# Kernel tuning notes

Measured on AMD Instinct MI355X. Metric: run time of the kernel, lower is better.

The kernel has to match this reference:

```python
import jax, jax.numpy as jnp
import numpy as np

R = 9  # kernal for deep=1


def setup_inputs() -> dict:
    key = jax.random.key(0)
    ks = jax.random.split(key, 9)
    B, Cin, Cout, H, W = 4, 128, 128, 360, 360
    r2 = R * R
    x = jax.random.normal(ks[0], (B, Cin, H, W), dtype=jnp.float32)
    Wconv = jax.random.normal(ks[1], (Cout, Cin), dtype=jnp.float32) * 0.05
    bconv = jax.random.normal(ks[2], (Cout,), dtype=jnp.float32) * 0.05
    Wa = jax.random.normal(ks[3], (r2, r2), dtype=jnp.float32) * 0.05
    ba = jax.random.normal(ks[4], (r2,), dtype=jnp.float32) * 0.05
    Wb = jax.random.normal(ks[5], (r2, r2), dtype=jnp.float32) * 0.05
    bb = jax.random.normal(ks[6], (r2,), dtype=jnp.float32) * 0.05
    Wc = jax.random.normal(ks[7], (r2, r2), dtype=jnp.float32) * 0.05
    bc = jax.random.normal(ks[8], (r2,), dtype=jnp.float32) * 0.05
    return {"x": x, "Wconv": Wconv, "bconv": bconv,
            "Wa": Wa, "ba": ba, "Wb": Wb, "bb": bb, "Wc": Wc, "bc": bc}


def reference(x, Wconv, bconv, Wa, ba, Wb, bb, Wc, bc):
    r = R
    # 1x1 conv == channel-mixing matmul
    x = jnp.einsum('bchw,oc->bohw', x, Wconv) + bconv[None, :, None, None]
    B, C, H, W = x.shape
    padh = (-H) % r
    padw = (-W) % r
    x = jnp.pad(x, ((0, 0), (0, 0), (0, padh), (0, padw)))
    Hp, Wp = H + padh, W + padw
    h, w = Hp // r, Wp // r
    # rearrange 'b c (ch h) (cw w) -> b c (h w) (ch cw)', ch=cw=r
    x = x.reshape(B, C, r, h, r, w).transpose(0, 1, 3, 5, 2, 4).reshape(B, C, h * w, r * r)
    a = x @ Wa.T + ba
    b = x @ Wb.T + bb
    c = x @ Wc.T + bc
    # linear-attention trick: a @ (b^T @ c); b^T@c is (r^2, r^2) per (b,c)
    y = a @ (jnp.swapaxes(b, -1, -2) @ c) / r
    # inverse rearrange 'b c (h w) (ch cw) -> b c (ch h) (cw w)'
    y = y.reshape(B, C, h, w, r, r).transpose(0, 1, 4, 2, 5, 3).reshape(B, C, Hp, Wp)
    return y[:, :, :Hp - padh, :Wp - padw]
```

## Files before the change

### kernel.cpp

```cpp
#include <hip/hip_runtime.h>
#include <hip/hip_bf16.h>

typedef float f32x4 __attribute__((ext_vector_type(4)));
typedef short s16x8 __attribute__((ext_vector_type(8)));

#define DEVI __device__ __forceinline__

DEVI unsigned short f2bf(float f) {
    return __builtin_bit_cast(unsigned short, __float2bfloat16(f));
}


__global__ __launch_bounds__(256) void k_prep(
    const float* __restrict__ W, const float* __restrict__ Wa,
    const float* __restrict__ ba, const float* __restrict__ Wb,
    const float* __restrict__ bb, const float* __restrict__ Wc,
    const float* __restrict__ bc, unsigned short* __restrict__ Wbf,
    float* __restrict__ EAT, float* __restrict__ WCAT)
{
    const int tid = threadIdx.x, bid = blockIdx.x;
    if (bid < 64) {
        const int i = bid * 256 + tid;
        Wbf[i] = f2bf(W[i]);
        return;
    }
    const int out = (bid - 64) * 256 + tid;
    const int row = out / 96, col = out % 96;
    float ea = 0.f;
    if (row <= 81 && col <= 81) {
        for (int p = 0; p < 81; ++p) {
            const float wa = (col < 81) ? Wa[p * 81 + col] : ba[p];
            const float wb = (row < 81) ? Wb[p * 81 + row] : bb[p];
            ea += wa * wb;
        }
    }
    EAT[out] = ea;
    float wc = 0.f;
    if (col < 81) {
        if (row < 81) wc = Wc[col * 81 + row];
        else if (row == 81) wc = bc[col];
    }
    WCAT[out] = wc;
}

__global__ __launch_bounds__(256, 3) void k_conv(
    const float* __restrict__ x, const unsigned short* __restrict__ Wbf,
    const float* __restrict__ bcv, unsigned short* __restrict__ XR)
{
    __shared__ __align__(16) unsigned short Xs[160 * 136];
    const int tid = threadIdx.x;
    int bid = blockIdx.x;
    const int rb = bid % 10; bid /= 10;
    const int cw = bid % 9;  bid /= 9;
    const int ch = bid % 9;  const int b = bid / 9;
    const int H0 = ch * 40 + rb * 4, w0 = cw * 40;
    const int kfeat = ch * 9 + cw;
    const int t0 = rb * 160;

    const float* xb = x + (size_t)b * 128 * 129600;
    float4 va[5][4];
#pragma unroll
    for (int ii = 0; ii < 5; ++ii) {
        const int i = tid + ii * 256;
        const int cq = i / 40, nq = i % 40;
        const int hh = nq / 10, sub = nq % 10;
        const float* p = xb + (size_t)(cq * 4) * 129600 + (size_t)(H0 + hh) * 360 + w0 + sub * 4;
        va[ii][0] = *reinterpret_cast<const float4*>(p);
        va[ii][1] = *reinterpret_cast<const float4*>(p + 129600);
        va[ii][2] = *reinterpret_cast<const float4*>(p + 2 * 129600);
        va[ii][3] = *reinterpret_cast<const float4*>(p + 3 * 129600);
    }
#pragma unroll
    for (int ii = 0; ii < 5; ++ii) {
        const int i = tid + ii * 256;
        const int cq = i / 40, nq = i % 40;
        const int hh = nq / 10, sub = nq % 10;
        const int n0 = hh * 40 + sub * 4;
        const int cs = (cq ^ ((((n0 >> 2)) & 7) << 1)) * 4;
        const float4 v0 = va[ii][0], v1 = va[ii][1], v2 = va[ii][2], v3 = va[ii][3];
        ushort4 w0v = { f2bf(v0.x), f2bf(v1.x), f2bf(v2.x), f2bf(v3.x) };
        ushort4 w1v = { f2bf(v0.y), f2bf(v1.y), f2bf(v2.y), f2bf(v3.y) };
        ushort4 w2v = { f2bf(v0.z), f2bf(v1.z), f2bf(v2.z), f2bf(v3.z) };
        ushort4 w3v = { f2bf(v0.w), f2bf(v1.w), f2bf(v2.w), f2bf(v3.w) };
        *reinterpret_cast<ushort4*>(&Xs[(n0 + 0) * 136 + cs]) = w0v;
        *reinterpret_cast<ushort4*>(&Xs[(n0 + 1) * 136 + cs]) = w1v;
        *reinterpret_cast<ushort4*>(&Xs[(n0 + 2) * 136 + cs]) = w2v;
        *reinterpret_cast<ushort4*>(&Xs[(n0 + 3) * 136 + cs]) = w3v;
    }
    __syncthreads();

    const int lane = tid & 63, wid = tid >> 6;
    const int wm = wid >> 1, wn = wid & 1;
    const int lr = lane & 15, lg = lane >> 4;

    f32x4 acc[5][4] = {};
#pragma unroll
    for (int kk = 0; kk < 4; ++kk) {
        s16x8 xa[5], wb[4];
#pragma unroll
        for (int at = 0; at < 5; ++at) {
            const int n = wm * 80 + at * 16 + lr;
            const int cqs = ((kk * 8 + lg * 2) ^ (((n >> 2) & 7) << 1)) * 4;
            xa[at] = *reinterpret_cast<const s16x8*>(&Xs[n * 136 + cqs]);
        }
#pragma unroll
        for (int bt = 0; bt < 4; ++bt)
            wb[bt] = *reinterpret_cast<const s16x8*>(
                Wbf + (wn * 64 + bt * 16 + lr) * 128 + kk * 32 + lg * 8);
#pragma unroll
        for (int at = 0; at < 5; ++at)
#pragma unroll
            for (int bt = 0; bt < 4; ++bt)
                acc[at][bt] = __builtin_amdgcn_mfma_f32_16x16x32_bf16(xa[at], wb[bt], acc[at][bt], 0, 0, 0);
    }
    __syncthreads();
#pragma unroll
    for (int bt = 0; bt < 4; ++bt) {
        const int o = wn * 64 + bt * 16 + lr;
        const float bias = bcv[o];
#pragma unroll
        for (int at = 0; at < 5; ++at) {
            const int n0 = wm * 80 + at * 16 + lg * 4;
            ushort4 hv = { f2bf(acc[at][bt][0] + bias), f2bf(acc[at][bt][1] + bias),
                           f2bf(acc[at][bt][2] + bias), f2bf(acc[at][bt][3] + bias) };
            *reinterpret_cast<ushort4*>(&Xs[o * 168 + n0]) = hv;
        }
    }
    __syncthreads();
    unsigned short* dstb = XR + (size_t)b * 128 * 129600 + (size_t)kfeat * 1600 + t0;
#pragma unroll
    for (int j = 0; j < 10; ++j) {
        const int item = tid + j * 256;
        const int o = item / 20, s2 = item % 20;
        *reinterpret_cast<s16x8*>(dstb + (size_t)o * 129600 + s2 * 8) =
            *reinterpret_cast<const s16x8*>(&Xs[o * 168 + s2 * 8]);
    }
}

__global__ __launch_bounds__(256) void k_gram(
    const unsigned short* __restrict__ XR, float* __restrict__ G2)
{
    __shared__ __align__(16) unsigned short Rs[96 * 168];
    const int tid = threadIdx.x;
    const int half = blockIdx.x & 1, bo = blockIdx.x >> 1;
    for (int i = 81 * 168 + tid; i < 96 * 168; i += 256)
        Rs[i] = (i < 82 * 168) ? (unsigned short)0x3F80 : (unsigned short)0;
    const unsigned short* Rg = XR + (size_t)bo * 129600;
    const int lane = tid & 63, wid = tid >> 6;
    const int wm = wid >> 1, wn = wid & 1;
    const int lr = lane & 15, lg = lane >> 4;
    f32x4 acc[3][3] = {};
    for (int it = 0; it < 5; ++it) {
        const int t0 = half * 800 + it * 160;
        __syncthreads();
        for (int i = tid; i < 81 * 20; i += 256) {
            const int r = i / 20, g = i % 20;
            *reinterpret_cast<s16x8*>(&Rs[r * 168 + g * 8]) =
                *reinterpret_cast<const s16x8*>(Rg + (size_t)r * 1600 + t0 + g * 8);
        }
        __syncthreads();
#pragma unroll
        for (int kk = 0; kk < 5; ++kk) {
            const int koff = kk * 32 + lg * 8;
            s16x8 af[3], bfr[3];
#pragma unroll
            for (int mt = 0; mt < 3; ++mt)
                af[mt] = *reinterpret_cast<const s16x8*>(&Rs[(wm * 48 + mt * 16 + lr) * 168 + koff]);
#pragma unroll
            for (int nt = 0; nt < 3; ++nt)
                bfr[nt] = *reinterpret_cast<const s16x8*>(&Rs[(wn * 48 + nt * 16 + lr) * 168 + koff]);
#pragma unroll
            for (int mt = 0; mt < 3; ++mt)
#pragma unroll
                for (int nt = 0; nt < 3; ++nt)
                    acc[mt][nt] = __builtin_amdgcn_mfma_f32_16x16x32_bf16(af[mt], bfr[nt], acc[mt][nt], 0, 0, 0);
        }
    }
    float* Gb = G2 + (size_t)(half * 512 + bo) * 9216;
#pragma unroll
    for (int mt = 0; mt < 3; ++mt)
#pragma unroll
        for (int nt = 0; nt < 3; ++nt)
#pragma unroll
            for (int rg = 0; rg < 4; ++rg) {
                const int row = wm * 48 + mt * 16 + lg * 4 + rg;
                const int col = wn * 48 + nt * 16 + lr;
                Gb[row * 96 + col] = acc[mt][nt][rg];
            }
}

__global__ __launch_bounds__(256) void k_small(
    const float* __restrict__ G2, const float* __restrict__ EAT,
    const float* __restrict__ WCAT, unsigned short* __restrict__ NT)
{
    __shared__ float Gs[96 * 98];
    __shared__ float Us[96 * 98];
    const int tid = threadIdx.x;
    const int bo = blockIdx.x;
    const int ty = tid >> 4, tx = tid & 15;
    const int r0 = ty * 6, q0 = tx * 6;

    const float* Gg0 = G2 + (size_t)bo * 9216;
    const float* Gg1 = G2 + (size_t)(512 + bo) * 9216;
    for (int i = tid; i < 96 * 96; i += 256) {
        const int r = i / 96, c = i % 96;
        Gs[r * 98 + c] = Gg0[i] + Gg1[i];
    }
    __syncthreads();

    {
        float acc[6][6] = {};
        for (int l = 0; l <= 81; ++l) {
            float gv[6], wv[6];
#pragma unroll
            for (int a = 0; a < 6; ++a) gv[a] = Gs[l * 98 + r0 + a];
#pragma unroll
            for (int b2 = 0; b2 < 6; ++b2) wv[b2] = WCAT[l * 96 + q0 + b2];
#pragma unroll
            for (int a = 0; a < 6; ++a)
#pragma unroll
                for (int b2 = 0; b2 < 6; ++b2)
                    acc[a][b2] += gv[a] * wv[b2];
        }
#pragma unroll
        for (int a = 0; a < 6; ++a)
#pragma unroll
            for (int b2 = 0; b2 < 6; ++b2)
                Us[(r0 + a) * 98 + q0 + b2] = acc[a][b2];
    }
    __syncthreads();

    float acc[6][6] = {};
    for (int j = 0; j <= 81; ++j) {
        float ev[6], uv[6];
#pragma unroll
        for (int a = 0; a < 6; ++a) ev[a] = EAT[j * 96 + r0 + a];
#pragma unroll
        for (int b2 = 0; b2 < 6; ++b2) uv[b2] = Us[j * 98 + q0 + b2];
#pragma unroll
        for (int a = 0; a < 6; ++a)
#pragma unroll
            for (int b2 = 0; b2 < 6; ++b2)
                acc[a][b2] += ev[a] * uv[b2];
    }
    unsigned short* NTb = NT + (size_t)bo * 9216;
#pragma unroll
    for (int b2 = 0; b2 < 6; ++b2)
#pragma unroll
        for (int a = 0; a < 6; ++a)
            NTb[(q0 + b2) * 96 + (r0 + a)] = f2bf(acc[a][b2] * (1.f / 9.f));
}

__global__ __launch_bounds__(256) void k_apply(
    const unsigned short* __restrict__ XR, const unsigned short* __restrict__ NT,
    float* __restrict__ out)
{
    __shared__ __align__(16) unsigned short Xs[160 * 128];
    const int tid = threadIdx.x;
    const int fifth = blockIdx.x % 5, bo = blockIdx.x / 5;
    for (int i = tid; i < 320; i += 256) {
        const int t = i >> 1, h = i & 1;
        const int s = (t >> 3) & 7;
        const ushort4 z = { 0, 0, 0, 0 };
        if (h == 0) {
            *reinterpret_cast<ushort4*>(&Xs[t * 128 + ((10 ^ s) << 3) + 4]) = z;
        } else {
            *reinterpret_cast<ushort4*>(&Xs[t * 128 + ((11 ^ s) << 3)]) = z;
            *reinterpret_cast<ushort4*>(&Xs[t * 128 + ((11 ^ s) << 3) + 4]) = z;
        }
    }
    const int lane = tid & 63, wid = tid >> 6;
    const int wm = wid >> 1, wn = wid & 1;
    const int lr = lane & 15, lg = lane >> 4;

    const unsigned short* NTb = NT + (size_t)bo * 9216;
    s16x8 nb[3][3];
#pragma unroll
    for (int qt = 0; qt < 3; ++qt)
#pragma unroll
        for (int kk = 0; kk < 3; ++kk)
            nb[qt][kk] = *reinterpret_cast<const s16x8*>(
                NTb + (wn * 48 + qt * 16 + lr) * 96 + kk * 32 + lg * 8);

    const unsigned short* Rg = XR + (size_t)bo * 129600;
    float* ob = out + (size_t)bo * 129600;

    for (int it = 0; it < 2; ++it) {
        const int t0 = fifth * 320 + it * 160;
        __syncthreads();
        for (int i = tid; i < 420; i += 256) {
            const int kq = i / 20, g = i % 20;
            if (kq < 20) {
                const unsigned short* src = Rg + (size_t)(4 * kq) * 1600 + t0 + g * 8;
                const s16x8 v0 = *reinterpret_cast<const s16x8*>(src);
                const s16x8 v1 = *reinterpret_cast<const s16x8*>(src + 1600);
                const s16x8 v2 = *reinterpret_cast<const s16x8*>(src + 3200);
                const s16x8 v3 = *reinterpret_cast<const s16x8*>(src + 4800);
                const int colb = (((kq >> 1) ^ (g & 7)) << 3) + ((kq & 1) << 2);
#pragma unroll
                for (int e = 0; e < 8; ++e) {
                    const int t = g * 8 + e;
                    ushort4 wv = { (unsigned short)v0[e], (unsigned short)v1[e],
                                   (unsigned short)v2[e], (unsigned short)v3[e] };
                    *reinterpret_cast<ushort4*>(&Xs[t * 128 + colb]) = wv;
                }
            } else {
                const s16x8 v = *reinterpret_cast<const s16x8*>(
                    Rg + (size_t)80 * 1600 + t0 + g * 8);
                const int colb = (10 ^ (g & 7)) << 3;
#pragma unroll
                for (int e = 0; e < 8; ++e) {
                    const int t = g * 8 + e;
                    ushort4 wv = { (unsigned short)v[e], (unsigned short)0x3F80, 0, 0 };
                    *reinterpret_cast<ushort4*>(&Xs[t * 128 + colb]) = wv;
                }
            }
        }
        __syncthreads();
        f32x4 acc[5][3] = {};
#pragma unroll
        for (int kk = 0; kk < 3; ++kk) {
            s16x8 xa[5];
#pragma unroll
            for (int at = 0; at < 5; ++at) {
                const int t = wm * 80 + at * 16 + lr;
                const int s = (t >> 3) & 7;
                xa[at] = *reinterpret_cast<const s16x8*>(
                    &Xs[t * 128 + (((kk * 4 + lg) ^ s) << 3)]);
            }
#pragma unroll
            for (int at = 0; at < 5; ++at)
#pragma unroll
                for (int qt = 0; qt < 3; ++qt)
                    acc[at][qt] = __builtin_amdgcn_mfma_f32_16x16x32_bf16(xa[at], nb[qt][kk], acc[at][qt], 0, 0, 0);
        }
#pragma unroll
        for (int qt = 0; qt < 3; ++qt) {
            const int q = wn * 48 + qt * 16 + lr;
            if (q < 81) {
                const int chq = q / 9, cwq = q % 9;
                float* oq = ob + (size_t)chq * 40 * 360 + cwq * 40;
#pragma unroll
                for (int at = 0; at < 5; ++at) {
                    const int tt = t0 + wm * 80 + at * 16 + lg * 4;
                    const int hh = tt / 40, ww = tt % 40;
                    *reinterpret_cast<f32x4*>(&oq[hh * 360 + ww]) = acc[at][qt];
                }
            }
        }
    }
}

extern "C" void kernel_launch(void* const* d_in, const int* in_sizes, int n_in,
                              void* d_out, int out_size, void* d_ws, size_t ws_size,
                              hipStream_t stream)
{
    (void)in_sizes; (void)n_in; (void)out_size; (void)ws_size;
    const float* x   = (const float*)d_in[0];
    const float* Wcv = (const float*)d_in[1];
    const float* bcv = (const float*)d_in[2];
    const float* Wa  = (const float*)d_in[3];
    const float* ba  = (const float*)d_in[4];
    const float* Wb  = (const float*)d_in[5];
    const float* bbv = (const float*)d_in[6];
    const float* Wc  = (const float*)d_in[7];
    const float* bc2 = (const float*)d_in[8];
    float* out = (float*)d_out;

    char* w = (char*)d_ws;
    unsigned short* XR = (unsigned short*)w;
    float* G2 = (float*)(w + 132710400ull);
    unsigned short* NT = (unsigned short*)(w + 170459136ull);
    unsigned short* Wbf = (unsigned short*)(w + 179896320ull);
    float* EAT  = (float*)(w + 179929088ull);
    float* WCAT = (float*)(w + 179965952ull);

    k_prep <<<100,  256, 0, stream>>>(Wcv, Wa, ba, Wb, bbv, Wc, bc2, Wbf, EAT, WCAT);
    k_conv <<<3240, 256, 0, stream>>>(x, Wbf, bcv, XR);
    k_gram <<<1024, 256, 0, stream>>>(XR, G2);
    k_small<<<512,  256, 0, stream>>>(G2, EAT, WCAT, NT);
    k_apply<<<2560, 256, 0, stream>>>(XR, NT, out);
}
```

Before: 305.5 us.

## Software-pipeline global loads in conv and apply kernels with register prefetch

k_conv now processes two row-blocks per workgroup and issues the second block's global loads before computing the first, halving the grid and lowering occupancy to 2 waves per SIMD. k_apply processes five 160-column tiles per block instead of two, with a register double-buffer that prefetches the next tile's XR data while MFMAs run on the current one. The aim is to hide global memory latency behind compute. The cost is higher register pressure and fewer blocks, which can reduce latency hiding from occupancy.

```diff
diff --git a/kernel.cpp b/kernel.cpp
--- a/kernel.cpp
+++ b/kernel.cpp
@@ -43,22 +43,8 @@
     WCAT[out] = wc;
 }
 
-__global__ __launch_bounds__(256, 3) void k_conv(
-    const float* __restrict__ x, const unsigned short* __restrict__ Wbf,
-    const float* __restrict__ bcv, unsigned short* __restrict__ XR)
-{
-    __shared__ __align__(16) unsigned short Xs[160 * 136];
-    const int tid = threadIdx.x;
-    int bid = blockIdx.x;
-    const int rb = bid % 10; bid /= 10;
-    const int cw = bid % 9;  bid /= 9;
-    const int ch = bid % 9;  const int b = bid / 9;
-    const int H0 = ch * 40 + rb * 4, w0 = cw * 40;
-    const int kfeat = ch * 9 + cw;
-    const int t0 = rb * 160;
-
-    const float* xb = x + (size_t)b * 128 * 129600;
-    float4 va[5][4];
+DEVI void conv_issue(const float* xb, int H0, int w0, int tid, float4 (&va)[5][4])
+{
 #pragma unroll
     for (int ii = 0; ii < 5; ++ii) {
         const int i = tid + ii * 256;
@@ -70,6 +56,10 @@
         va[ii][2] = *reinterpret_cast<const float4*>(p + 2 * 129600);
         va[ii][3] = *reinterpret_cast<const float4*>(p + 3 * 129600);
     }
+}
+
+DEVI void conv_stage(const float4 (&va)[5][4], unsigned short* Xs, int tid)
+{
 #pragma unroll
     for (int ii = 0; ii < 5; ++ii) {
         const int i = tid + ii * 256;
@@ -87,8 +77,11 @@
         *reinterpret_cast<ushort4*>(&Xs[(n0 + 2) * 136 + cs]) = w2v;
         *reinterpret_cast<ushort4*>(&Xs[(n0 + 3) * 136 + cs]) = w3v;
     }
-    __syncthreads();
-
+}
+
+DEVI void conv_compute_store(unsigned short* Xs, const unsigned short* __restrict__ Wbf,
+                             const float* __restrict__ bcv, unsigned short* dstb, int tid)
+{
     const int lane = tid & 63, wid = tid >> 6;
     const int wm = wid >> 1, wn = wid & 1;
     const int lr = lane & 15, lg = lane >> 4;
@@ -127,7 +120,6 @@
         }
     }
     __syncthreads();
-    unsigned short* dstb = XR + (size_t)b * 128 * 129600 + (size_t)kfeat * 1600 + t0;
 #pragma unroll
     for (int j = 0; j < 10; ++j) {
         const int item = tid + j * 256;
@@ -135,6 +127,37 @@
         *reinterpret_cast<s16x8*>(dstb + (size_t)o * 129600 + s2 * 8) =
             *reinterpret_cast<const s16x8*>(&Xs[o * 168 + s2 * 8]);
     }
+    __syncthreads();
+}
+
+__global__ __launch_bounds__(256, 2) void k_conv(
+    const float* __restrict__ x, const unsigned short* __restrict__ Wbf,
+    const float* __restrict__ bcv, unsigned short* __restrict__ XR)
+{
+    __shared__ __align__(16) unsigned short Xs[160 * 136];
+    const int tid = threadIdx.x;
+    int bid = blockIdx.x;
+    const int rb2 = bid % 5; bid /= 5;
+    const int cw = bid % 9;  bid /= 9;
+    const int ch = bid % 9;  const int b = bid / 9;
+    const int w0 = cw * 40;
+    const int kfeat = ch * 9 + cw;
+    const int rb0 = rb2 * 2;
+    const int H0a = ch * 40 + rb0 * 4;
+
+    const float* xb = x + (size_t)b * 128 * 129600;
+    unsigned short* dst0 = XR + (size_t)(b * 128) * 129600 + (size_t)kfeat * 1600;
+
+    float4 va[5][4], vb[5][4];
+    conv_issue(xb, H0a, w0, tid, va);
+    conv_stage(va, Xs, tid);
+    __syncthreads();
+    conv_issue(xb, H0a + 4, w0, tid, vb);
+    conv_compute_store(Xs, Wbf, bcv, dst0 + rb0 * 160, tid);
+
+    conv_stage(vb, Xs, tid);
+    __syncthreads();
+    conv_compute_store(Xs, Wbf, bcv, dst0 + (rb0 + 1) * 160, tid);
 }
 
 __global__ __launch_bounds__(256) void k_gram(
@@ -251,13 +274,77 @@
             NTb[(q0 + b2) * 96 + (r0 + a)] = f2bf(acc[a][b2] * (1.f / 9.f));
 }
 
+DEVI void apply_issue(const unsigned short* Rg, int t0, int tid, s16x8 (&pf)[2][4])
+{
+    {
+        const int kq = tid / 20, g = tid % 20;
+        const unsigned short* src = Rg + (size_t)(4 * kq) * 1600 + t0 + g * 8;
+        pf[0][0] = *reinterpret_cast<const s16x8*>(src);
+        pf[0][1] = *reinterpret_cast<const s16x8*>(src + 1600);
+        pf[0][2] = *reinterpret_cast<const s16x8*>(src + 3200);
+        pf[0][3] = *reinterpret_cast<const s16x8*>(src + 4800);
+    }
+    if (tid < 164) {
+        const int item = tid + 256;
+        const int kq = item / 20, g = item % 20;
+        if (kq < 20) {
+            const unsigned short* src = Rg + (size_t)(4 * kq) * 1600 + t0 + g * 8;
+            pf[1][0] = *reinterpret_cast<const s16x8*>(src);
+            pf[1][1] = *reinterpret_cast<const s16x8*>(src + 1600);
+            pf[1][2] = *reinterpret_cast<const s16x8*>(src + 3200);
+            pf[1][3] = *reinterpret_cast<const s16x8*>(src + 4800);
+        } else {
+            pf[1][0] = *reinterpret_cast<const s16x8*>(
+                Rg + (size_t)80 * 1600 + t0 + g * 8);
+        }
+    }
+}
+
+DEVI void apply_stage(int tid, const s16x8 (&pf)[2][4], unsigned short* Xs)
+{
+    {
+        const int kq = tid / 20, g = tid % 20;
+        const int colb = (((kq >> 1) ^ (g & 7)) << 3) + ((kq & 1) << 2);
+#pragma unroll
+        for (int e = 0; e < 8; ++e) {
+            const int t = g * 8 + e;
+            ushort4 wv = { (unsigned short)pf[0][0][e], (unsigned short)pf[0][1][e],
+                           (unsigned short)pf[0][2][e], (unsigned short)pf[0][3][e] };
+            *reinterpret_cast<ushort4*>(&Xs[t * 128 + colb]) = wv;
+        }
+    }
+    if (tid < 164) {
+        const int item = tid + 256;
+        const int kq = item / 20, g = item % 20;
+        if (kq < 20) {
+            const int colb = (((kq >> 1) ^ (g & 7)) << 3) + ((kq & 1) << 2);
+#pragma unroll
+            for (int e = 0; e < 8; ++e) {
+                const int t = g * 8 + e;
+                ushort4 wv = { (unsigned short)pf[1][0][e], (unsigned short)pf[1][1][e],
+                               (unsigned short)pf[1][2][e], (unsigned short)pf[1][3][e] };
+                *reinterpret_cast<ushort4*>(&Xs[t * 128 + colb]) = wv;
+            }
+        } else {
+            const int colb = (10 ^ (g & 7)) << 3;
+#pragma unroll
+            for (int e = 0; e < 8; ++e) {
+                const int t = g * 8 + e;
+                ushort4 wv = { (unsigned short)pf[1][0][e], (unsigned short)0x3F80, 0, 0 };
+                *reinterpret_cast<ushort4*>(&Xs[t * 128 + colb]) = wv;
+            }
+        }
+    }
+}
+
 __global__ __launch_bounds__(256) void k_apply(
     const unsigned short* __restrict__ XR, const unsigned short* __restrict__ NT,
     float* __restrict__ out)
 {
     __shared__ __align__(16) unsigned short Xs[160 * 128];
     const int tid = threadIdx.x;
-    const int fifth = blockIdx.x % 5, bo = blockIdx.x / 5;
+    const int half = blockIdx.x & 1, bo = blockIdx.x >> 1;
+    const int t00 = half * 800;
     for (int i = tid; i < 320; i += 256) {
         const int t = i >> 1, h = i & 1;
         const int s = (t >> 3) & 7;
@@ -285,38 +372,16 @@
     const unsigned short* Rg = XR + (size_t)bo * 129600;
     float* ob = out + (size_t)bo * 129600;
 
-    for (int it = 0; it < 2; ++it) {
-        const int t0 = fifth * 320 + it * 160;
+    s16x8 pf[2][2][4];
+    apply_issue(Rg, t00, tid, pf[0]);
+
+#pragma unroll
+    for (int it = 0; it < 5; ++it) {
+        const int t0 = t00 + it * 160;
+        apply_stage(tid, pf[it & 1], Xs);
         __syncthreads();
-        for (int i = tid; i < 420; i += 256) {
-            const int kq = i / 20, g = i % 20;
-            if (kq < 20) {
-                const unsigned short* src = Rg + (size_t)(4 * kq) * 1600 + t0 + g * 8;
-                const s16x8 v0 = *reinterpret_cast<const s16x8*>(src);
-                const s16x8 v1 = *reinterpret_cast<const s16x8*>(src + 1600);
-                const s16x8 v2 = *reinterpret_cast<const s16x8*>(src + 3200);
-                const s16x8 v3 = *reinterpret_cast<const s16x8*>(src + 4800);
-                const int colb = (((kq >> 1) ^ (g & 7)) << 3) + ((kq & 1) << 2);
-#pragma unroll
-                for (int e = 0; e < 8; ++e) {
-                    const int t = g * 8 + e;
-                    ushort4 wv = { (unsigned short)v0[e], (unsigned short)v1[e],
-                                   (unsigned short)v2[e], (unsigned short)v3[e] };
-                    *reinterpret_cast<ushort4*>(&Xs[t * 128 + colb]) = wv;
-                }
-            } else {
-                const s16x8 v = *reinterpret_cast<const s16x8*>(
-                    Rg + (size_t)80 * 1600 + t0 + g * 8);
-                const int colb = (10 ^ (g & 7)) << 3;
-#pragma unroll
-                for (int e = 0; e < 8; ++e) {
-                    const int t = g * 8 + e;
-                    ushort4 wv = { (unsigned short)v[e], (unsigned short)0x3F80, 0, 0 };
-                    *reinterpret_cast<ushort4*>(&Xs[t * 128 + colb]) = wv;
-                }
-            }
-        }
-        __syncthreads();
+        if (it < 4)
+            apply_issue(Rg, t0 + 160, tid, pf[(it & 1) ^ 1]);
         f32x4 acc[5][3] = {};
 #pragma unroll
         for (int kk = 0; kk < 3; ++kk) {
@@ -348,6 +413,7 @@
                 }
             }
         }
+        __syncthreads();
     }
 }
 
@@ -376,8 +442,8 @@
     float* WCAT = (float*)(w + 179965952ull);
 
     k_prep <<<100,  256, 0, stream>>>(Wcv, Wa, ba, Wb, bbv, Wc, bc2, Wbf, EAT, WCAT);
-    k_conv <<<3240, 256, 0, stream>>>(x, Wbf, bcv, XR);
+    k_conv <<<1620, 256, 0, stream>>>(x, Wbf, bcv, XR);
     k_gram <<<1024, 256, 0, stream>>>(XR, G2);
     k_small<<<512,  256, 0, stream>>>(G2, EAT, WCAT, NT);
-    k_apply<<<2560, 256, 0, stream>>>(XR, NT, out);
-}
+    k_apply<<<1024, 256, 0, stream>>>(XR, NT, out);
+}
```

New measurement: 363.5 us. 1.19x slower.

## Split conv input staging into two channel halves overlapping loads with MFMA

Applied to the files above, without the earlier changes.

Splits the k_conv global-to-LDS staging into two halves of 64 input channels. The second half's global loads are issued before the first half's MFMA loop runs, and are converted and written to shared memory afterwards. This hides part of the global load latency behind compute. It costs extra register pressure to hold the in-flight loads under launch bounds of 3 blocks per SM, plus one added barrier.

```diff
diff --git a/kernel.cpp b/kernel.cpp
--- a/kernel.cpp
+++ b/kernel.cpp
@@ -58,44 +58,63 @@
     const int t0 = rb * 160;
 
     const float* xb = x + (size_t)b * 128 * 129600;
-    float4 va[5][4];
-#pragma unroll
-    for (int ii = 0; ii < 5; ++ii) {
-        const int i = tid + ii * 256;
-        const int cq = i / 40, nq = i % 40;
-        const int hh = nq / 10, sub = nq % 10;
-        const float* p = xb + (size_t)(cq * 4) * 129600 + (size_t)(H0 + hh) * 360 + w0 + sub * 4;
-        va[ii][0] = *reinterpret_cast<const float4*>(p);
-        va[ii][1] = *reinterpret_cast<const float4*>(p + 129600);
-        va[ii][2] = *reinterpret_cast<const float4*>(p + 2 * 129600);
-        va[ii][3] = *reinterpret_cast<const float4*>(p + 3 * 129600);
-    }
-#pragma unroll
-    for (int ii = 0; ii < 5; ++ii) {
-        const int i = tid + ii * 256;
-        const int cq = i / 40, nq = i % 40;
-        const int hh = nq / 10, sub = nq % 10;
-        const int n0 = hh * 40 + sub * 4;
-        const int cs = (cq ^ ((((n0 >> 2)) & 7) << 1)) * 4;
-        const float4 v0 = va[ii][0], v1 = va[ii][1], v2 = va[ii][2], v3 = va[ii][3];
-        ushort4 w0v = { f2bf(v0.x), f2bf(v1.x), f2bf(v2.x), f2bf(v3.x) };
-        ushort4 w1v = { f2bf(v0.y), f2bf(v1.y), f2bf(v2.y), f2bf(v3.y) };
-        ushort4 w2v = { f2bf(v0.z), f2bf(v1.z), f2bf(v2.z), f2bf(v3.z) };
-        ushort4 w3v = { f2bf(v0.w), f2bf(v1.w), f2bf(v2.w), f2bf(v3.w) };
-        *reinterpret_cast<ushort4*>(&Xs[(n0 + 0) * 136 + cs]) = w0v;
-        *reinterpret_cast<ushort4*>(&Xs[(n0 + 1) * 136 + cs]) = w1v;
-        *reinterpret_cast<ushort4*>(&Xs[(n0 + 2) * 136 + cs]) = w2v;
-        *reinterpret_cast<ushort4*>(&Xs[(n0 + 3) * 136 + cs]) = w3v;
-    }
-    __syncthreads();
-
     const int lane = tid & 63, wid = tid >> 6;
     const int wm = wid >> 1, wn = wid & 1;
     const int lr = lane & 15, lg = lane >> 4;
 
+    float4 va[3][4];
+#pragma unroll
+    for (int ii = 0; ii < 3; ++ii) {
+        const int i = tid + ii * 256;
+        if (i < 640) {
+            const int cq = i / 40, nq = i % 40;
+            const int hh = nq / 10, sub = nq % 10;
+            const float* p = xb + (size_t)(cq * 4) * 129600 + (size_t)(H0 + hh) * 360 + w0 + sub * 4;
+            va[ii][0] = *reinterpret_cast<const float4*>(p);
+            va[ii][1] = *reinterpret_cast<const float4*>(p + 129600);
+            va[ii][2] = *reinterpret_cast<const float4*>(p + 2 * 129600);
+            va[ii][3] = *reinterpret_cast<const float4*>(p + 3 * 129600);
+        }
+    }
+#pragma unroll
+    for (int ii = 0; ii < 3; ++ii) {
+        const int i = tid + ii * 256;
+        if (i < 640) {
+            const int cq = i / 40, nq = i % 40;
+            const int hh = nq / 10, sub = nq % 10;
+            const int n0 = hh * 40 + sub * 4;
+            const int cs = (cq ^ ((((n0 >> 2)) & 7) << 1)) * 4;
+            const float4 v0 = va[ii][0], v1 = va[ii][1], v2 = va[ii][2], v3 = va[ii][3];
+            ushort4 w0v = { f2bf(v0.x), f2bf(v1.x), f2bf(v2.x), f2bf(v3.x) };
+            ushort4 w1v = { f2bf(v0.y), f2bf(v1.y), f2bf(v2.y), f2bf(v3.y) };
+            ushort4 w2v = { f2bf(v0.z), f2bf(v1.z), f2bf(v2.z), f2bf(v3.z) };
+            ushort4 w3v = { f2bf(v0.w), f2bf(v1.w), f2bf(v2.w), f2bf(v3.w) };
+            *reinterpret_cast<ushort4*>(&Xs[(n0 + 0) * 136 + cs]) = w0v;
+            *reinterpret_cast<ushort4*>(&Xs[(n0 + 1) * 136 + cs]) = w1v;
+            *reinterpret_cast<ushort4*>(&Xs[(n0 + 2) * 136 + cs]) = w2v;
+            *reinterpret_cast<ushort4*>(&Xs[(n0 + 3) * 136 + cs]) = w3v;
+        }
+    }
+    __syncthreads();
+
+    float4 vb[3][4];
+#pragma unroll
+    for (int ii = 0; ii < 3; ++ii) {
+        const int i = tid + ii * 256;
+        if (i < 640) {
+            const int cq = 16 + i / 40, nq = i % 40;
+            const int hh = nq / 10, sub = nq % 10;
+            const float* p = xb + (size_t)(cq * 4) * 129600 + (size_t)(H0 + hh) * 360 + w0 + sub * 4;
+            vb[ii][0] = *reinterpret_cast<const float4*>(p);
+            vb[ii][1] = *reinterpret_cast<const float4*>(p + 129600);
+            vb[ii][2] = *reinterpret_cast<const float4*>(p + 2 * 129600);
+            vb[ii][3] = *reinterpret_cast<const float4*>(p + 3 * 129600);
+        }
+    }
+
     f32x4 acc[5][4] = {};
 #pragma unroll
-    for (int kk = 0; kk < 4; ++kk) {
+    for (int kk = 0; kk < 2; ++kk) {
         s16x8 xa[5], wb[4];
 #pragma unroll
         for (int at = 0; at < 5; ++at) {
@@ -113,6 +132,48 @@
             for (int bt = 0; bt < 4; ++bt)
                 acc[at][bt] = __builtin_amdgcn_mfma_f32_16x16x32_bf16(xa[at], wb[bt], acc[at][bt], 0, 0, 0);
     }
+
+#pragma unroll
+    for (int ii = 0; ii < 3; ++ii) {
+        const int i = tid + ii * 256;
+        if (i < 640) {
+            const int cq = 16 + i / 40, nq = i % 40;
+            const int hh = nq / 10, sub = nq % 10;
+            const int n0 = hh * 40 + sub * 4;
+            const int cs = (cq ^ ((((n0 >> 2)) & 7) << 1)) * 4;
+            const float4 v0 = vb[ii][0], v1 = vb[ii][1], v2 = vb[ii][2], v3 = vb[ii][3];
+            ushort4 w0v = { f2bf(v0.x), f2bf(v1.x), f2bf(v2.x), f2bf(v3.x) };
+            ushort4 w1v = { f2bf(v0.y), f2bf(v1.y), f2bf(v2.y), f2bf(v3.y) };
+            ushort4 w2v = { f2bf(v0.z), f2bf(v1.z), f2bf(v2.z), f2bf(v3.z) };
+            ushort4 w3v = { f2bf(v0.w), f2bf(v1.w), f2bf(v2.w), f2bf(v3.w) };
+            *reinterpret_cast<ushort4*>(&Xs[(n0 + 0) * 136 + cs]) = w0v;
+            *reinterpret_cast<ushort4*>(&Xs[(n0 + 1) * 136 + cs]) = w1v;
+            *reinterpret_cast<ushort4*>(&Xs[(n0 + 2) * 136 + cs]) = w2v;
+            *reinterpret_cast<ushort4*>(&Xs[(n0 + 3) * 136 + cs]) = w3v;
+        }
+    }
+    __syncthreads();
+
+#pragma unroll
+    for (int kk = 2; kk < 4; ++kk) {
+        s16x8 xa[5], wb[4];
+#pragma unroll
+        for (int at = 0; at < 5; ++at) {
+            const int n = wm * 80 + at * 16 + lr;
+            const int cqs = ((kk * 8 + lg * 2) ^ (((n >> 2) & 7) << 1)) * 4;
+            xa[at] = *reinterpret_cast<const s16x8*>(&Xs[n * 136 + cqs]);
+        }
+#pragma unroll
+        for (int bt = 0; bt < 4; ++bt)
+            wb[bt] = *reinterpret_cast<const s16x8*>(
+                Wbf + (wn * 64 + bt * 16 + lr) * 128 + kk * 32 + lg * 8);
+#pragma unroll
+        for (int at = 0; at < 5; ++at)
+#pragma unroll
+            for (int bt = 0; bt < 4; ++bt)
+                acc[at][bt] = __builtin_amdgcn_mfma_f32_16x16x32_bf16(xa[at], wb[bt], acc[at][bt], 0, 0, 0);
+    }
+
     __syncthreads();
 #pragma unroll
     for (int bt = 0; bt < 4; ++bt) {
```

Measured after the change: 369.3 us. 1.21x slower.

## Fuse Gram accumulation and small-matrix stage into one kernel

Applied to the files above, without the earlier changes.

Merges k_gram and k_small into a single kernel that computes the full Gram matrix per (batch, channel) over all tiles, keeps it in shared memory, and then runs the two small matmuls to produce NT. This removes the G2 global round trip, the split-half reduction and one kernel launch. In exchange the Gram stage runs with 512 blocks instead of 1024, each doing twice the serial work, and shared memory is aliased between Rs and Us, which adds extra barriers.

```diff
diff --git a/kernel.cpp b/kernel.cpp
--- a/kernel.cpp
+++ b/kernel.cpp
@@ -137,21 +137,27 @@
     }
 }
 
-__global__ __launch_bounds__(256) void k_gram(
-    const unsigned short* __restrict__ XR, float* __restrict__ G2)
-{
-    __shared__ __align__(16) unsigned short Rs[96 * 168];
+__global__ __launch_bounds__(256) void k_gs(
+    const unsigned short* __restrict__ XR, const float* __restrict__ EAT,
+    const float* __restrict__ WCAT, unsigned short* __restrict__ NT)
+{
+    __shared__ __align__(16) char smem[37632 + 37632];
+    float* Gs = reinterpret_cast<float*>(smem);
+    unsigned short* Rs = reinterpret_cast<unsigned short*>(smem + 37632);
+    float* Us = reinterpret_cast<float*>(smem + 37632);
+
     const int tid = threadIdx.x;
-    const int half = blockIdx.x & 1, bo = blockIdx.x >> 1;
+    const int bo = blockIdx.x;
     for (int i = 81 * 168 + tid; i < 96 * 168; i += 256)
         Rs[i] = (i < 82 * 168) ? (unsigned short)0x3F80 : (unsigned short)0;
     const unsigned short* Rg = XR + (size_t)bo * 129600;
     const int lane = tid & 63, wid = tid >> 6;
     const int wm = wid >> 1, wn = wid & 1;
     const int lr = lane & 15, lg = lane >> 4;
+
     f32x4 acc[3][3] = {};
-    for (int it = 0; it < 5; ++it) {
-        const int t0 = half * 800 + it * 160;
+    for (int it = 0; it < 10; ++it) {
+        const int t0 = it * 160;
         __syncthreads();
         for (int i = tid; i < 81 * 20; i += 256) {
             const int r = i / 20, g = i % 20;
@@ -176,7 +182,7 @@
                     acc[mt][nt] = __builtin_amdgcn_mfma_f32_16x16x32_bf16(af[mt], bfr[nt], acc[mt][nt], 0, 0, 0);
         }
     }
-    float* Gb = G2 + (size_t)(half * 512 + bo) * 9216;
+    __syncthreads();
 #pragma unroll
     for (int mt = 0; mt < 3; ++mt)
 #pragma unroll
@@ -185,31 +191,15 @@
             for (int rg = 0; rg < 4; ++rg) {
                 const int row = wm * 48 + mt * 16 + lg * 4 + rg;
                 const int col = wn * 48 + nt * 16 + lr;
-                Gb[row * 96 + col] = acc[mt][nt][rg];
+                Gs[row * 98 + col] = acc[mt][nt][rg];
             }
-}
-
-__global__ __launch_bounds__(256) void k_small(
-    const float* __restrict__ G2, const float* __restrict__ EAT,
-    const float* __restrict__ WCAT, unsigned short* __restrict__ NT)
-{
-    __shared__ float Gs[96 * 98];
-    __shared__ float Us[96 * 98];
-    const int tid = threadIdx.x;
-    const int bo = blockIdx.x;
+    __syncthreads();
+
     const int ty = tid >> 4, tx = tid & 15;
     const int r0 = ty * 6, q0 = tx * 6;
 
-    const float* Gg0 = G2 + (size_t)bo * 9216;
-    const float* Gg1 = G2 + (size_t)(512 + bo) * 9216;
-    for (int i = tid; i < 96 * 96; i += 256) {
-        const int r = i / 96, c = i % 96;
-        Gs[r * 98 + c] = Gg0[i] + Gg1[i];
-    }
-    __syncthreads();
-
     {
-        float acc[6][6] = {};
+        float a2[6][6] = {};
         for (int l = 0; l <= 81; ++l) {
             float gv[6], wv[6];
 #pragma unroll
@@ -220,17 +210,18 @@
             for (int a = 0; a < 6; ++a)
 #pragma unroll
                 for (int b2 = 0; b2 < 6; ++b2)
-                    acc[a][b2] += gv[a] * wv[b2];
-        }
+                    a2[a][b2] += gv[a] * wv[b2];
+        }
+        __syncthreads();
 #pragma unroll
         for (int a = 0; a < 6; ++a)
 #pragma unroll
             for (int b2 = 0; b2 < 6; ++b2)
-                Us[(r0 + a) * 98 + q0 + b2] = acc[a][b2];
-    }
-    __syncthreads();
-
-    float acc[6][6] = {};
+                Us[(r0 + a) * 98 + q0 + b2] = a2[a][b2];
+    }
+    __syncthreads();
+
+    float a3[6][6] = {};
     for (int j = 0; j <= 81; ++j) {
         float ev[6], uv[6];
 #pragma unroll
@@ -241,14 +232,14 @@
         for (int a = 0; a < 6; ++a)
 #pragma unroll
             for (int b2 = 0; b2 < 6; ++b2)
-                acc[a][b2] += ev[a] * uv[b2];
+                a3[a][b2] += ev[a] * uv[b2];
     }
     unsigned short* NTb = NT + (size_t)bo * 9216;
 #pragma unroll
     for (int b2 = 0; b2 < 6; ++b2)
 #pragma unroll
         for (int a = 0; a < 6; ++a)
-            NTb[(q0 + b2) * 96 + (r0 + a)] = f2bf(acc[a][b2] * (1.f / 9.f));
+            NTb[(q0 + b2) * 96 + (r0 + a)] = f2bf(a3[a][b2] * (1.f / 9.f));
 }
 
 __global__ __launch_bounds__(256) void k_apply(
@@ -369,7 +360,6 @@
 
     char* w = (char*)d_ws;
     unsigned short* XR = (unsigned short*)w;
-    float* G2 = (float*)(w + 132710400ull);
     unsigned short* NT = (unsigned short*)(w + 170459136ull);
     unsigned short* Wbf = (unsigned short*)(w + 179896320ull);
     float* EAT  = (float*)(w + 179929088ull);
@@ -377,7 +367,6 @@
 
     k_prep <<<100,  256, 0, stream>>>(Wcv, Wa, ba, Wb, bbv, Wc, bc2, Wbf, EAT, WCAT);
     k_conv <<<3240, 256, 0, stream>>>(x, Wbf, bcv, XR);
-    k_gram <<<1024, 256, 0, stream>>>(XR, G2);
-    k_small<<<512,  256, 0, stream>>>(G2, EAT, WCAT, NT);
+    k_gs   <<<512,  256, 0, stream>>>(XR, EAT, WCAT, NT);
     k_apply<<<2560, 256, 0, stream>>>(XR, NT, out);
 }
```

Measured after the change: 303.6 us. Within noise of the previous version (-0.6%).
